# Optimization experiments

Hardware: AMD Instinct MI355X
Metric: run time of the kernel (lower is better)

Reference implementation:

```python
import jax, jax.numpy as jnp
import numpy as np

B, P, D = 256, 128, 768        # batch, property slots per sample, encoder hidden dim
E = 64                          # num_properties (number of adapter heads)
H = 256                         # adapter_hidden_dim
H2 = H // 2
O = 2                           # output_dim
LN_EPS = 1e-5
RES_W_ADPT, RES_W_BASE = 0.7, 0.3


def setup_inputs() -> dict:
    key = jax.random.key(0)
    ks = jax.random.split(key, 12)
    hidden_states = jax.random.normal(ks[0], (B, P, D), dtype=jnp.float32)
    base_output = jax.random.normal(ks[1], (B, P, O), dtype=jnp.float32)
    properties = jax.random.randint(ks[2], (B, P), 0, E, dtype=jnp.int64)
    mask = (jax.random.uniform(ks[3], (B, P)) > 0.1).astype(jnp.float32)
    # Stacked per-head adapter parameters (LayerNorm + 3 Linears per head)
    ln_g = jnp.ones((E, D), dtype=jnp.float32)
    ln_b = jnp.zeros((E, D), dtype=jnp.float32)
    W1 = jax.random.normal(ks[4], (E, D, H), dtype=jnp.float32) * (1.0 / np.sqrt(D))
    b1 = jnp.zeros((E, H), dtype=jnp.float32)
    W2 = jax.random.normal(ks[5], (E, H, H2), dtype=jnp.float32) * (1.0 / np.sqrt(H))
    b2 = jnp.zeros((E, H2), dtype=jnp.float32)
    W3 = jax.random.normal(ks[6], (E, H2, O), dtype=jnp.float32) * 0.01  # init std=0.01 per source
    b3 = jnp.zeros((E, O), dtype=jnp.float32)
    return {
        "hidden_states": hidden_states, "base_output": base_output,
        "properties": properties, "mask": mask,
        "ln_g": ln_g, "ln_b": ln_b, "W1": W1, "b1": b1,
        "W2": W2, "b2": b2, "W3": W3, "b3": b3,
    }


def reference(hidden_states, base_output, properties, mask,
              ln_g, ln_b, W1, b1, W2, b2, W3, b3):
    b, p, d = hidden_states.shape
    o = W3.shape[-1]
    x = hidden_states.reshape(-1, d)                        # [N, D]
    # LayerNorm statistics are head-independent; only gamma/beta differ per head
    mu = jnp.mean(x, axis=-1, keepdims=True)
    var = jnp.mean((x - mu) ** 2, axis=-1, keepdims=True)
    xhat = (x - mu) * jax.lax.rsqrt(var + LN_EPS)           # [N, D]
    flat_p = properties.reshape(-1)                         # [N]
    flat_m = mask.reshape(-1)                               # [N]

    def body(acc, inp):
        idx, g, bt, w1, bb1, w2, bb2, w3, bb3 = inp
        h = jax.nn.relu((xhat * g + bt) @ w1 + bb1)         # [N, H]  (dropout = identity in eval)
        h = jax.nn.relu(h @ w2 + bb2)                       # [N, H2]
        out = h @ w3 + bb3                                  # [N, O]
        sel = (flat_p == idx) & (flat_m > 0)
        return jnp.where(sel[:, None], out, acc), None

    e = W1.shape[0]
    acc0 = jnp.zeros((b * p, o), dtype=x.dtype)
    acc, _ = jax.lax.scan(
        body, acc0,
        (jnp.arange(e), ln_g, ln_b, W1, b1, W2, b2, W3, b3))
    out = acc.reshape(b, p, o)
    out = RES_W_ADPT * out + RES_W_BASE * base_output       # use_residual=True
    return out * mask[..., None]
```

## Files before the change

### kernel.cpp

```cpp
#include <hip/hip_runtime.h>
#include <stdint.h>

typedef unsigned short u16;
typedef unsigned int   u32;

#define NTOK   32768
#define GD     768
#define GH     256
#define GH2    128
#define GE     64

typedef __bf16 bf16x8 __attribute__((ext_vector_type(8)));
typedef float  f32x4  __attribute__((ext_vector_type(4)));
union Frag { uint4 u; bf16x8 b; };

__device__ __forceinline__ float bf2f(u16 h) {
  union { u32 u; float f; } v; v.u = ((u32)h) << 16; return v.f;
}
__device__ __forceinline__ u16 f2bf(float f) {
  union { float f; u32 u; } v; v.f = f;
  u32 r = (v.u + 0x7fffu + ((v.u >> 16) & 1u)) >> 16;
  return (u16)r;
}

__device__ __forceinline__ void async16(void* lds, const void* g) {
  __builtin_amdgcn_global_load_lds(
      (const __attribute__((address_space(1))) void*)g,
      (__attribute__((address_space(3))) void*)lds, 16, 0, 0);
}

__device__ __forceinline__ void bar_lds() {
  asm volatile("s_waitcnt lgkmcnt(0)" ::: "memory");
  __builtin_amdgcn_sched_barrier(0);
  __builtin_amdgcn_s_barrier();
  __builtin_amdgcn_sched_barrier(0);
}

__device__ __forceinline__ int getProp(const int* p32, int t, int is64) {
  return is64 ? p32[2 * t] : p32[t];
}

static const size_t OFF_W1T  = 0;
static const size_t OFF_W2T  = 25165824;
static const size_t OFF_TOK  = 29360128;
static const size_t OFF_META = 29491200;

__global__ void setup_kernel(const int* __restrict__ prop, const float* __restrict__ mask,
                             u32* __restrict__ outz, int* __restrict__ counts2d,
                             int* __restrict__ cursors_p, int* __restrict__ flagp) {
  __shared__ int h[GE];
  __shared__ int vOr;
  const int b = blockIdx.x;
  const int tid = threadIdx.x;
  outz[b * 512 + tid] = 0u;
  outz[b * 512 + 256 + tid] = 0u;
  if (b < 4) cursors_p[b * 256 + tid] = 0;
  if (tid < GE) h[tid] = 0;
  if (tid == 0) vOr = 0;
  __syncthreads();
  int v = prop[2 * tid + 1] | prop[2 * (tid + 256) + 1];
  if (v) atomicOr(&vOr, 1);
  __syncthreads();
  const int is64 = (vOr == 0) ? 1 : 0;
  if (b == 0 && tid == 0) *flagp = is64;
  const int t = b * 256 + tid;
  if (mask[t] > 0.f) atomicAdd(&h[getProp(prop, t, is64)], 1);
  __syncthreads();
  if (tid < GE) counts2d[b * GE + tid] = h[tid];
}

__global__ void transpose_w1(const float* __restrict__ in, u16* __restrict__ out) {
  __shared__ u16 tl[64][260];
  const int bid = blockIdx.x;
  const int e  = bid / 12, r = bid % 12;
  const int d0 = (r / 4) * 256, h0 = (r % 4) * 64;
  const int tid = threadIdx.x;
  const size_t inMat = (size_t)e * GD * GH;
  const size_t outMat = (size_t)e * GH * GD;
  const int h_l = (tid & 15) * 4, d_l = tid >> 4;
#pragma unroll
  for (int dd = 0; dd < 16; ++dd) {
    const int d = d_l + dd * 16;
    float4 v = *(const float4*)(in + inMat + (size_t)(d0 + d) * GH + h0 + h_l);
    tl[h_l + 0][d] = f2bf(v.x);
    tl[h_l + 1][d] = f2bf(v.y);
    tl[h_l + 2][d] = f2bf(v.z);
    tl[h_l + 3][d] = f2bf(v.w);
  }
  __syncthreads();
  const int wv = tid >> 6, ln = tid & 63;
  const int d_glob = d0 + ln * 4;
  const size_t tbase = outMat + (size_t)(d_glob >> 5) * 8192 +
                       (size_t)((d_glob >> 3) & 3) * 2048 + (d_glob & 7);
#pragma unroll
  for (int hh = 0; hh < 16; ++hh) {
    const int h = wv * 16 + hh;
    *(uint2*)(out + tbase + (size_t)(h0 + h) * 8) = *(const uint2*)&tl[h][ln * 4];
  }
}

__global__ void transpose_w2(const float* __restrict__ in, u16* __restrict__ out) {
  __shared__ u16 tile[32][33];
  const int tilesPerMat = 32;
  const int e  = blockIdx.x / tilesPerMat;
  const int t  = blockIdx.x % tilesPerMat;
  const int tr = t / 4, tc = t % 4;
  const size_t mat = (size_t)e * GH * GH2;
  const int tx = threadIdx.x & 31, ty = threadIdx.x >> 5;
  const int r0 = tr * 32, c0 = tc * 32;
#pragma unroll
  for (int i = 0; i < 32; i += 8)
    tile[ty + i][tx] = f2bf(in[mat + (size_t)(r0 + ty + i) * GH2 + c0 + tx]);
  __syncthreads();
  const int k = r0 + tx;
  const size_t kbase = mat + (size_t)(k >> 5) * 4096 +
                       (size_t)((k >> 3) & 3) * 1024 + (k & 7);
#pragma unroll
  for (int i = 0; i < 32; i += 8)
    out[kbase + (size_t)(c0 + ty + i) * 8] = tile[tx][ty + i];
}

__global__ void scan_kernel(const int* __restrict__ counts2d, int* __restrict__ offsets,
                            int* __restrict__ tileHead, int* __restrict__ tileRow,
                            int* __restrict__ nTilesPtr) {
  __shared__ int part[4][GE];
  const int tid = threadIdx.x;
  const int e = tid & 63, q = tid >> 6;
  int c = 0;
  for (int b = q * 32; b < q * 32 + 32; ++b) c += counts2d[b * GE + e];
  part[q][e] = c;
  __syncthreads();
  if (tid < GE) {
    const int ct = part[0][e] + part[1][e] + part[2][e] + part[3][e];
    int inc = ct;
#pragma unroll
    for (int d = 1; d < 64; d <<= 1) { int n = __shfl_up(inc, d); if (e >= d) inc += n; }
    const int off = inc - ct;
    offsets[e] = off;
    if (e == 63) offsets[64] = inc;
    int ntile = (ct + 63) >> 6;
    int inct = ntile;
#pragma unroll
    for (int d = 1; d < 64; d <<= 1) { int n = __shfl_up(inct, d); if (e >= d) inct += n; }
    const int tb = inct - ntile;
    for (int j = 0; j < ntile; ++j) { tileHead[tb + j] = e; tileRow[tb + j] = off + j * 64; }
    if (e == 63) *nTilesPtr = inct;
  }
}

__global__ void scatter_kernel(const int* __restrict__ prop, const float* __restrict__ mask,
                               const int* __restrict__ offsets, int* __restrict__ cursors_p,
                               int* __restrict__ tokenIds, const int* __restrict__ flag) {
  __shared__ int h[GE];
  __shared__ int basebin[GE];
  const int tid = threadIdx.x;
  const int t = blockIdx.x * 256 + tid;
  if (tid < GE) h[tid] = 0;
  __syncthreads();
  int p = -1, rank = 0;
  if (mask[t] > 0.f) {
    p = getProp(prop, t, *flag);
    rank = atomicAdd(&h[p], 1);
  }
  __syncthreads();
  if (tid < GE && h[tid] > 0) basebin[tid] = atomicAdd(&cursors_p[tid * 16], h[tid]);
  __syncthreads();
  if (p >= 0) tokenIds[offsets[p] + basebin[p] + rank] = t;
}

__global__ __launch_bounds__(256, 2) void adapter_gemm(
    const float* __restrict__ hs, const u16* __restrict__ w1t, const u16* __restrict__ w2t,
    const float* __restrict__ lng, const float* __restrict__ lnb,
    const float* __restrict__ b1, const float* __restrict__ b2,
    const float* __restrict__ w3, const float* __restrict__ b3,
    const float* __restrict__ base, const float* __restrict__ mask,
    const int* __restrict__ tokenIds, const int* __restrict__ offsets,
    const int* __restrict__ tileHead, const int* __restrict__ tileRow,
    const int* __restrict__ nTilesPtr, float* __restrict__ outp) {
  __shared__ union LU {
    struct { u16 A[3][2048]; u16 B[3][8192]; } s;
    u16 h[17408];
  } uni;
  __shared__ float sBias1[256];
  __shared__ float sBias2[128];
  __shared__ float sW3[2][128];
  __shared__ float sB3[2];
  __shared__ int   sTok[64];
  __shared__ __align__(16) float sGam[GD];
  __shared__ __align__(16) float sBet[GD];
  __shared__ float sMu[64];
  __shared__ float sRstd[64];

  const int tid  = threadIdx.x;
  const int wv   = tid >> 6;
  const int ln   = tid & 63;
  const int l15  = tid & 15;
  const int quad = (tid & 63) >> 4;
  const f32x4 vzero = {0.f, 0.f, 0.f, 0.f};
  const int nt = *nTilesPtr;
  const int qq = nt >> 3, rr = nt & 7;

  for (int i = blockIdx.x; i < nt; i += gridDim.x) {
    const int x = i & 7, s = i >> 3;
    const int tile = (x < rr ? x * (qq + 1) : rr * (qq + 1) + (x - rr) * qq) + s;

    __syncthreads();
    const int e  = tileHead[tile];
    const int rs = tileRow[tile];
    const int nRows = min(64, offsets[e + 1] - rs);

    if (tid < 64) sTok[tid] = tokenIds[rs + min(tid, nRows - 1)];
    sBias1[tid] = b1[e * GH + tid];
    if (tid < 128) sBias2[tid] = b2[e * GH2 + tid];
    { const int k = tid >> 1, o = tid & 1; sW3[o][k] = w3[e * GH2 * 2 + k * 2 + o]; }
    if (tid < 2) sB3[tid] = b3[e * 2 + tid];
    __syncthreads();

    const u16* w1e = w1t + (size_t)e * GH * GD;
    const u16* w2e = w2t + (size_t)e * GH2 * GH;

    if (tid < 192) {
      *(float4*)&sGam[tid * 4] = *(const float4*)(lng + (size_t)e * GD + tid * 4);
      *(float4*)&sBet[tid * 4] = *(const float4*)(lnb + (size_t)e * GD + tid * 4);
    }

    const int r0  = tid >> 3;
    const int klo = (tid & 7) * 4;
    const int kgrp = klo >> 3, kin = klo & 7;
    const float* xA = hs + (size_t)sTok[r0] * GD + klo;
    const float* xB = hs + (size_t)sTok[r0 + 32] * GD + klo;

#define ISSUE_B(S, KT) do {                                                     \
    u16* _bb = uni.s.B[S] + wv * 2048;                                          \
    const u16* _gg = w1e + (KT) * 8192 + wv * 2048 + ln * 8;                    \
    async16(_bb,        _gg);        async16(_bb + 512,  _gg + 512);            \
    async16(_bb + 1024, _gg + 1024); async16(_bb + 1536, _gg + 1536);           \
  } while (0)

    float4 pAa[2], pAb[2];
    ISSUE_B(0, 0);
    __builtin_amdgcn_sched_barrier(0);
    pAa[0] = *(const float4*)(xA);
    pAb[0] = *(const float4*)(xB);
    ISSUE_B(1, 1);
    __builtin_amdgcn_sched_barrier(0);
    pAa[1] = *(const float4*)(xA + 32);
    pAb[1] = *(const float4*)(xB + 32);

#pragma unroll 2
    for (int pass = 0; pass < 4; ++pass) {
      const int row = pass * 16 + (tid >> 4);
      const int l16 = tid & 15;
      const float* xp = hs + (size_t)sTok[row] * GD + l16 * 4;
      float sm = 0.f, sq = 0.f;
#pragma unroll
      for (int c = 0; c < 12; ++c) {
        float4 u = *(const float4*)(xp + c * 64);
        sm += u.x + u.y + u.z + u.w;
        sq += u.x*u.x + u.y*u.y + u.z*u.z + u.w*u.w;
      }
#pragma unroll
      for (int d = 1; d < 16; d <<= 1) { sm += __shfl_xor(sm, d); sq += __shfl_xor(sq, d); }
      if (l16 == 0) {
        const float mu = sm * (1.f / 768.f);
        sMu[row] = mu;
        sRstd[row] = rsqrtf(sq * (1.f / 768.f) - mu * mu + 1e-5f);
      }
    }
    bar_lds();

    const float muA = sMu[r0],      rsA = sRstd[r0];
    const float muB = sMu[r0 + 32], rsB = sRstd[r0 + 32];

#define XFORM_WRITE(PAR, AA, BB, K0) do {                                       \
    const float4 gv = *(const float4*)&sGam[(K0) + klo];                        \
    const float4 bv = *(const float4*)&sBet[(K0) + klo];                        \
    uint2 oa, ob;                                                               \
    oa.x = (u32)f2bf((AA.x - muA) * rsA * gv.x + bv.x)                          \
         | ((u32)f2bf((AA.y - muA) * rsA * gv.y + bv.y) << 16);                 \
    oa.y = (u32)f2bf((AA.z - muA) * rsA * gv.z + bv.z)                          \
         | ((u32)f2bf((AA.w - muA) * rsA * gv.w + bv.w) << 16);                 \
    ob.x = (u32)f2bf((BB.x - muB) * rsB * gv.x + bv.x)                          \
         | ((u32)f2bf((BB.y - muB) * rsB * gv.y + bv.y) << 16);                 \
    ob.y = (u32)f2bf((BB.z - muB) * rsB * gv.z + bv.z)                          \
         | ((u32)f2bf((BB.w - muB) * rsB * gv.w + bv.w) << 16);                 \
    *(uint2*)&uni.s.A[PAR][kgrp * 512 + r0 * 8 + kin] = oa;                     \
    *(uint2*)&uni.s.A[PAR][kgrp * 512 + (r0 + 32) * 8 + kin] = ob;              \
  } while (0)

    XFORM_WRITE(0, pAa[0], pAb[0], 0);
    bar_lds();

    f32x4 acc1[4][4];
#pragma unroll
    for (int f = 0; f < 4; ++f)
#pragma unroll
      for (int g = 0; g < 4; ++g) acc1[f][g] = vzero;

#pragma unroll
    for (int kt = 0; kt < 24; ++kt) {
      const int par = kt % 3;
      Frag fa[4], fb[4];
#pragma unroll
      for (int f = 0; f < 4; ++f)
        fa[f].u = *(const uint4*)&uni.s.A[par][quad * 512 + (f * 16 + l15) * 8];
#pragma unroll
      for (int g = 0; g < 4; ++g)
        fb[g].u = *(const uint4*)&uni.s.B[par][quad * 2048 + (wv * 64 + g * 16 + l15) * 8];
      if (kt + 2 < 24) {
        ISSUE_B((kt + 2) % 3, kt + 2);
        __builtin_amdgcn_sched_barrier(0);
        pAa[kt & 1] = *(const float4*)(xA + (kt + 2) * 32);
        pAb[kt & 1] = *(const float4*)(xB + (kt + 2) * 32);
      }
#pragma unroll
      for (int f = 0; f < 4; ++f)
#pragma unroll
        for (int g = 0; g < 4; ++g)
          acc1[f][g] = __builtin_amdgcn_mfma_f32_16x16x32_bf16(fa[f].b, fb[g].b, acc1[f][g], 0, 0, 0);
      if (kt + 1 < 24)
        XFORM_WRITE((kt + 1) % 3, pAa[(kt + 1) & 1], pAb[(kt + 1) & 1], (kt + 1) * 32);
      if (kt < 22) {
        asm volatile("s_waitcnt vmcnt(6)" ::: "memory");
      } else {
        asm volatile("s_waitcnt vmcnt(0)" ::: "memory");
      }
      __builtin_amdgcn_sched_barrier(0);
      bar_lds();
    }
    bar_lds();

    Frag bW2[8][2];
#pragma unroll
    for (int kt = 0; kt < 8; ++kt)
#pragma unroll
      for (int g = 0; g < 2; ++g)
        bW2[kt][g].u = *(const uint4*)(w2e + kt * 4096 + quad * 1024 +
                                       (size_t)(wv * 32 + g * 16 + l15) * 8);

#pragma unroll
    for (int f = 0; f < 4; ++f)
#pragma unroll
      for (int g = 0; g < 4; ++g) {
        const int col = wv * 64 + g * 16 + l15;
        const float bias = sBias1[col];
#pragma unroll
        for (int r = 0; r < 4; ++r) {
          const int row = f * 16 + quad * 4 + r;
          uni.h[row * 264 + col] = f2bf(fmaxf(acc1[f][g][r] + bias, 0.f));
        }
      }
    bar_lds();

    f32x4 acc2[4][2];
#pragma unroll
    for (int f = 0; f < 4; ++f)
#pragma unroll
      for (int g = 0; g < 2; ++g) acc2[f][g] = vzero;

#pragma unroll
    for (int kt = 0; kt < 8; ++kt) {
      Frag fa2[4];
#pragma unroll
      for (int f = 0; f < 4; ++f)
        fa2[f].u = *(const uint4*)&uni.h[(f * 16 + l15) * 264 + kt * 32 + quad * 8];
#pragma unroll
      for (int f = 0; f < 4; ++f)
#pragma unroll
        for (int g = 0; g < 2; ++g)
          acc2[f][g] = __builtin_amdgcn_mfma_f32_16x16x32_bf16(fa2[f].b, bW2[kt][g].b, acc2[f][g], 0, 0, 0);
    }
    bar_lds();

#pragma unroll
    for (int f = 0; f < 4; ++f)
#pragma unroll
      for (int g = 0; g < 2; ++g) {
        const int col = wv * 32 + g * 16 + l15;
        const float bias = sBias2[col];
#pragma unroll
        for (int r = 0; r < 4; ++r) {
          const int row = f * 16 + quad * 4 + r;
          uni.h[row * 130 + col] = f2bf(fmaxf(acc2[f][g][r] + bias, 0.f));
        }
      }
    bar_lds();

    const int m = tid >> 1, o = tid & 1;
    if (m < nRows) {
      float a = sB3[o];
      const u16* h2row = &uni.h[m * 130];
#pragma unroll 16
      for (int k = 0; k < 128; ++k) a += bf2f(h2row[k]) * sW3[o][k];
      const int t = sTok[m];
      const float mk = mask[t];
      const float bs = base[t * 2 + o];
      outp[t * 2 + o] = (0.7f * a + 0.3f * bs) * mk;
    }
  }
#undef XFORM_WRITE
#undef ISSUE_B
}

extern "C" void kernel_launch(void* const* d_in, const int* in_sizes, int n_in,
                              void* d_out, int out_size, void* d_ws, size_t ws_size,
                              hipStream_t stream) {
  const float* hs   = (const float*)d_in[0];
  const float* base = (const float*)d_in[1];
  const int*   prop = (const int*)d_in[2];
  const float* mask = (const float*)d_in[3];
  const float* lng  = (const float*)d_in[4];
  const float* lnb  = (const float*)d_in[5];
  const float* W1   = (const float*)d_in[6];
  const float* b1   = (const float*)d_in[7];
  const float* W2   = (const float*)d_in[8];
  const float* b2   = (const float*)d_in[9];
  const float* W3   = (const float*)d_in[10];
  const float* b3   = (const float*)d_in[11];

  char* ws = (char*)d_ws;
  u16* w1t  = (u16*)(ws + OFF_W1T);
  u16* w2t  = (u16*)(ws + OFF_W2T);
  int* tok  = (int*)(ws + OFF_TOK);
  int* meta = (int*)(ws + OFF_META);
  int* counts2d  = meta;
  int* offsets   = meta + 8192;
  int* tileHead  = meta + 8320;
  int* tileRow   = meta + 9344;
  int* nTiles    = meta + 10368;
  int* propFlag  = meta + 10369;
  int* cursors_p = meta + 10432;

  setup_kernel<<<128, 256, 0, stream>>>(prop, mask, (u32*)d_out, counts2d,
                                        cursors_p, propFlag);
  transpose_w1<<<768, 256, 0, stream>>>(W1, w1t);
  transpose_w2<<<64 * 32, 256, 0, stream>>>(W2, w2t);
  scan_kernel<<<1, 256, 0, stream>>>(counts2d, offsets, tileHead, tileRow, nTiles);
  scatter_kernel<<<NTOK / 256, 256, 0, stream>>>(prop, mask, offsets, cursors_p, tok, propFlag);
  adapter_gemm<<<640, 256, 0, stream>>>(hs, w1t, w2t, lng, lnb, b1, b2, W3, b3,
                                        base, mask, tok, offsets, tileHead, tileRow,
                                        nTiles, (float*)d_out);
}
```

Measured before the change: 255.1 us.

## Use 128-row tiles with 512-thread blocks and a deeper W1 prefetch pipeline

Doubles the row tile from 64 to 128 tokens per head, so each W1/W2 weight slice is loaded once per 128 rows instead of per 64. Moves to 8 waves in a 2x4 row/column arrangement with 512-thread blocks, one block per CU, and 320 blocks. Deepens the prefetch pipeline to 4 B stages and 3 register stages for A, adds setprio around the MFMAs, and splits the final W3 dot product across lane pairs. The cost is more padding waste on partial tiles, lower occupancy, and higher LDS use.

```diff
diff --git a/kernel.cpp b/kernel.cpp
--- a/kernel.cpp
+++ b/kernel.cpp
@@ -138,12 +138,12 @@
     const int off = inc - ct;
     offsets[e] = off;
     if (e == 63) offsets[64] = inc;
-    int ntile = (ct + 63) >> 6;
+    int ntile = (ct + 127) >> 7;
     int inct = ntile;
 #pragma unroll
     for (int d = 1; d < 64; d <<= 1) { int n = __shfl_up(inct, d); if (e >= d) inct += n; }
     const int tb = inct - ntile;
-    for (int j = 0; j < ntile; ++j) { tileHead[tb + j] = e; tileRow[tb + j] = off + j * 64; }
+    for (int j = 0; j < ntile; ++j) { tileHead[tb + j] = e; tileRow[tb + j] = off + j * 128; }
     if (e == 63) *nTilesPtr = inct;
   }
 }
@@ -168,7 +168,7 @@
   if (p >= 0) tokenIds[offsets[p] + basebin[p] + rank] = t;
 }
 
-__global__ __launch_bounds__(256, 2) void adapter_gemm(
+__global__ __launch_bounds__(512, 1) void adapter_gemm(
     const float* __restrict__ hs, const u16* __restrict__ w1t, const u16* __restrict__ w2t,
     const float* __restrict__ lng, const float* __restrict__ lnb,
     const float* __restrict__ b1, const float* __restrict__ b2,
@@ -178,21 +178,23 @@
     const int* __restrict__ tileHead, const int* __restrict__ tileRow,
     const int* __restrict__ nTilesPtr, float* __restrict__ outp) {
   __shared__ union LU {
-    struct { u16 A[3][2048]; u16 B[3][8192]; } s;
-    u16 h[17408];
+    struct { u16 A[2][4096]; u16 B[4][8192]; } s;
+    u16 h[33792];
   } uni;
   __shared__ float sBias1[256];
   __shared__ float sBias2[128];
   __shared__ float sW3[2][128];
   __shared__ float sB3[2];
-  __shared__ int   sTok[64];
+  __shared__ int   sTok[128];
   __shared__ __align__(16) float sGam[GD];
   __shared__ __align__(16) float sBet[GD];
-  __shared__ float sMu[64];
-  __shared__ float sRstd[64];
+  __shared__ float sMu[128];
+  __shared__ float sRstd[128];
 
   const int tid  = threadIdx.x;
   const int wv   = tid >> 6;
+  const int wr   = wv >> 2;
+  const int wc   = wv & 3;
   const int ln   = tid & 63;
   const int l15  = tid & 15;
   const int quad = (tid & 63) >> 4;
@@ -207,12 +209,12 @@
     __syncthreads();
     const int e  = tileHead[tile];
     const int rs = tileRow[tile];
-    const int nRows = min(64, offsets[e + 1] - rs);
-
-    if (tid < 64) sTok[tid] = tokenIds[rs + min(tid, nRows - 1)];
-    sBias1[tid] = b1[e * GH + tid];
+    const int nRows = min(128, offsets[e + 1] - rs);
+
+    if (tid < 128) sTok[tid] = tokenIds[rs + min(tid, nRows - 1)];
+    if (tid < 256) sBias1[tid] = b1[e * GH + tid];
     if (tid < 128) sBias2[tid] = b2[e * GH2 + tid];
-    { const int k = tid >> 1, o = tid & 1; sW3[o][k] = w3[e * GH2 * 2 + k * 2 + o]; }
+    if (tid < 256) { const int k = tid >> 1, o = tid & 1; sW3[o][k] = w3[e * GH2 * 2 + k * 2 + o]; }
     if (tid < 2) sB3[tid] = b3[e * 2 + tid];
     __syncthreads();
 
@@ -224,32 +226,30 @@
       *(float4*)&sBet[tid * 4] = *(const float4*)(lnb + (size_t)e * GD + tid * 4);
     }
 
-    const int r0  = tid >> 3;
-    const int klo = (tid & 7) * 4;
-    const int kgrp = klo >> 3, kin = klo & 7;
-    const float* xA = hs + (size_t)sTok[r0] * GD + klo;
-    const float* xB = hs + (size_t)sTok[r0 + 32] * GD + klo;
-
-#define ISSUE_B(S, KT) do {                                                     \
-    u16* _bb = uni.s.B[S] + wv * 2048;                                          \
-    const u16* _gg = w1e + (KT) * 8192 + wv * 2048 + ln * 8;                    \
-    async16(_bb,        _gg);        async16(_bb + 512,  _gg + 512);            \
-    async16(_bb + 1024, _gg + 1024); async16(_bb + 1536, _gg + 1536);           \
+    const int r0x = tid >> 2;
+    const int kg  = tid & 3;
+    const int kg8 = kg * 8;
+    const float* xR = hs + (size_t)sTok[r0x] * GD + kg8;
+
+#define ISSUE_PA(D, KT) do {                                                    \
+    pA[D][0] = *(const float4*)(xR + (KT) * 32);                                \
+    pA[D][1] = *(const float4*)(xR + (KT) * 32 + 4);                            \
   } while (0)
 
-    float4 pAa[2], pAb[2];
+#define ISSUE_B(SB, KT) do {                                                    \
+    u16* _bb = uni.s.B[SB] + wv * 1024;                                         \
+    const u16* _gg = w1e + (KT) * 8192 + wv * 1024 + ln * 8;                    \
+    async16(_bb, _gg); async16(_bb + 512, _gg + 512);                           \
+  } while (0)
+
+    float4 pA[3][2];
+    ISSUE_PA(0, 0);
     ISSUE_B(0, 0);
     __builtin_amdgcn_sched_barrier(0);
-    pAa[0] = *(const float4*)(xA);
-    pAb[0] = *(const float4*)(xB);
-    ISSUE_B(1, 1);
-    __builtin_amdgcn_sched_barrier(0);
-    pAa[1] = *(const float4*)(xA + 32);
-    pAb[1] = *(const float4*)(xB + 32);
 
 #pragma unroll 2
     for (int pass = 0; pass < 4; ++pass) {
-      const int row = pass * 16 + (tid >> 4);
+      const int row = pass * 32 + (tid >> 4);
       const int l16 = tid & 15;
       const float* xp = hs + (size_t)sTok[row] * GD + l16 * 4;
       float sm = 0.f, sq = 0.f;
@@ -267,28 +267,36 @@
         sRstd[row] = rsqrtf(sq * (1.f / 768.f) - mu * mu + 1e-5f);
       }
     }
+    ISSUE_PA(1, 1);
+    ISSUE_B(1, 1);
+    ISSUE_PA(2, 2);
+    ISSUE_B(2, 2);
+    __builtin_amdgcn_sched_barrier(0);
     bar_lds();
 
-    const float muA = sMu[r0],      rsA = sRstd[r0];
-    const float muB = sMu[r0 + 32], rsB = sRstd[r0 + 32];
-
-#define XFORM_WRITE(PAR, AA, BB, K0) do {                                       \
-    const float4 gv = *(const float4*)&sGam[(K0) + klo];                        \
-    const float4 bv = *(const float4*)&sBet[(K0) + klo];                        \
-    uint2 oa, ob;                                                               \
-    oa.x = (u32)f2bf((AA.x - muA) * rsA * gv.x + bv.x)                          \
-         | ((u32)f2bf((AA.y - muA) * rsA * gv.y + bv.y) << 16);                 \
-    oa.y = (u32)f2bf((AA.z - muA) * rsA * gv.z + bv.z)                          \
-         | ((u32)f2bf((AA.w - muA) * rsA * gv.w + bv.w) << 16);                 \
-    ob.x = (u32)f2bf((BB.x - muB) * rsB * gv.x + bv.x)                          \
-         | ((u32)f2bf((BB.y - muB) * rsB * gv.y + bv.y) << 16);                 \
-    ob.y = (u32)f2bf((BB.z - muB) * rsB * gv.z + bv.z)                          \
-         | ((u32)f2bf((BB.w - muB) * rsB * gv.w + bv.w) << 16);                 \
-    *(uint2*)&uni.s.A[PAR][kgrp * 512 + r0 * 8 + kin] = oa;                     \
-    *(uint2*)&uni.s.A[PAR][kgrp * 512 + (r0 + 32) * 8 + kin] = ob;              \
+    const float muR = sMu[r0x], rsR = sRstd[r0x];
+
+#define XFORM_WRITE(PAR, D, K0) do {                                            \
+    const float4 g0 = *(const float4*)&sGam[(K0) + kg8];                        \
+    const float4 g1 = *(const float4*)&sGam[(K0) + kg8 + 4];                    \
+    const float4 bb0 = *(const float4*)&sBet[(K0) + kg8];                       \
+    const float4 bb1 = *(const float4*)&sBet[(K0) + kg8 + 4];                   \
+    const float4 va = pA[D][0], vb = pA[D][1];                                  \
+    uint4 o;                                                                    \
+    o.x = (u32)f2bf((va.x - muR) * rsR * g0.x + bb0.x)                          \
+        | ((u32)f2bf((va.y - muR) * rsR * g0.y + bb0.y) << 16);                 \
+    o.y = (u32)f2bf((va.z - muR) * rsR * g0.z + bb0.z)                          \
+        | ((u32)f2bf((va.w - muR) * rsR * g0.w + bb0.w) << 16);                 \
+    o.z = (u32)f2bf((vb.x - muR) * rsR * g1.x + bb1.x)                          \
+        | ((u32)f2bf((vb.y - muR) * rsR * g1.y + bb1.y) << 16);                 \
+    o.w = (u32)f2bf((vb.z - muR) * rsR * g1.z + bb1.z)                          \
+        | ((u32)f2bf((vb.w - muR) * rsR * g1.w + bb1.w) << 16);                 \
+    *(uint4*)&uni.s.A[PAR][kg * 1024 + r0x * 8] = o;                            \
   } while (0)
 
-    XFORM_WRITE(0, pAa[0], pAb[0], 0);
+    XFORM_WRITE(0, 0, 0);
+    asm volatile("s_waitcnt vmcnt(20)" ::: "memory");
+    __builtin_amdgcn_sched_barrier(0);
     bar_lds();
 
     f32x4 acc1[4][4];
@@ -299,36 +307,37 @@
 
 #pragma unroll
     for (int kt = 0; kt < 24; ++kt) {
-      const int par = kt % 3;
       Frag fa[4], fb[4];
 #pragma unroll
       for (int f = 0; f < 4; ++f)
-        fa[f].u = *(const uint4*)&uni.s.A[par][quad * 512 + (f * 16 + l15) * 8];
+        fa[f].u = *(const uint4*)&uni.s.A[kt & 1][quad * 1024 + (wr * 64 + f * 16 + l15) * 8];
 #pragma unroll
       for (int g = 0; g < 4; ++g)
-        fb[g].u = *(const uint4*)&uni.s.B[par][quad * 2048 + (wv * 64 + g * 16 + l15) * 8];
-      if (kt + 2 < 24) {
-        ISSUE_B((kt + 2) % 3, kt + 2);
+        fb[g].u = *(const uint4*)&uni.s.B[kt & 3][quad * 2048 + (wc * 64 + g * 16 + l15) * 8];
+      if (kt + 3 < 24) {
+        ISSUE_PA((kt + 3) % 3, kt + 3);
+        ISSUE_B((kt + 3) & 3, kt + 3);
         __builtin_amdgcn_sched_barrier(0);
-        pAa[kt & 1] = *(const float4*)(xA + (kt + 2) * 32);
-        pAb[kt & 1] = *(const float4*)(xB + (kt + 2) * 32);
-      }
+      }
+      __builtin_amdgcn_s_setprio(1);
 #pragma unroll
       for (int f = 0; f < 4; ++f)
 #pragma unroll
         for (int g = 0; g < 4; ++g)
           acc1[f][g] = __builtin_amdgcn_mfma_f32_16x16x32_bf16(fa[f].b, fb[g].b, acc1[f][g], 0, 0, 0);
+      __builtin_amdgcn_s_setprio(0);
       if (kt + 1 < 24)
-        XFORM_WRITE((kt + 1) % 3, pAa[(kt + 1) & 1], pAb[(kt + 1) & 1], (kt + 1) * 32);
-      if (kt < 22) {
-        asm volatile("s_waitcnt vmcnt(6)" ::: "memory");
-      } else {
+        XFORM_WRITE((kt + 1) & 1, (kt + 1) % 3, (kt + 1) * 32);
+      if (kt <= 20) {
+        asm volatile("s_waitcnt vmcnt(8)" ::: "memory");
+      } else if (kt == 21) {
+        asm volatile("s_waitcnt vmcnt(4)" ::: "memory");
+      } else if (kt == 22) {
         asm volatile("s_waitcnt vmcnt(0)" ::: "memory");
       }
       __builtin_amdgcn_sched_barrier(0);
       bar_lds();
     }
-    bar_lds();
 
     Frag bW2[8][2];
 #pragma unroll
@@ -336,17 +345,17 @@
 #pragma unroll
       for (int g = 0; g < 2; ++g)
         bW2[kt][g].u = *(const uint4*)(w2e + kt * 4096 + quad * 1024 +
-                                       (size_t)(wv * 32 + g * 16 + l15) * 8);
+                                       (size_t)(wc * 32 + g * 16 + l15) * 8);
 
 #pragma unroll
     for (int f = 0; f < 4; ++f)
 #pragma unroll
       for (int g = 0; g < 4; ++g) {
-        const int col = wv * 64 + g * 16 + l15;
+        const int col = wc * 64 + g * 16 + l15;
         const float bias = sBias1[col];
 #pragma unroll
         for (int r = 0; r < 4; ++r) {
-          const int row = f * 16 + quad * 4 + r;
+          const int row = wr * 64 + f * 16 + quad * 4 + r;
           uni.h[row * 264 + col] = f2bf(fmaxf(acc1[f][g][r] + bias, 0.f));
         }
       }
@@ -363,7 +372,7 @@
       Frag fa2[4];
 #pragma unroll
       for (int f = 0; f < 4; ++f)
-        fa2[f].u = *(const uint4*)&uni.h[(f * 16 + l15) * 264 + kt * 32 + quad * 8];
+        fa2[f].u = *(const uint4*)&uni.h[(wr * 64 + f * 16 + l15) * 264 + kt * 32 + quad * 8];
 #pragma unroll
       for (int f = 0; f < 4; ++f)
 #pragma unroll
@@ -376,29 +385,34 @@
     for (int f = 0; f < 4; ++f)
 #pragma unroll
       for (int g = 0; g < 2; ++g) {
-        const int col = wv * 32 + g * 16 + l15;
+        const int col = wc * 32 + g * 16 + l15;
         const float bias = sBias2[col];
 #pragma unroll
         for (int r = 0; r < 4; ++r) {
-          const int row = f * 16 + quad * 4 + r;
+          const int row = wr * 64 + f * 16 + quad * 4 + r;
           uni.h[row * 130 + col] = f2bf(fmaxf(acc2[f][g][r] + bias, 0.f));
         }
       }
     bar_lds();
 
-    const int m = tid >> 1, o = tid & 1;
-    if (m < nRows) {
-      float a = sB3[o];
-      const u16* h2row = &uni.h[m * 130];
+    {
+      const int m = tid >> 2, o = (tid >> 1) & 1, kh = tid & 1;
+      float a = (kh == 0) ? sB3[o] : 0.f;
+      const u16* h2row = &uni.h[m * 130 + kh * 64];
+      const float* w3row = &sW3[o][kh * 64];
 #pragma unroll 16
-      for (int k = 0; k < 128; ++k) a += bf2f(h2row[k]) * sW3[o][k];
-      const int t = sTok[m];
-      const float mk = mask[t];
-      const float bs = base[t * 2 + o];
-      outp[t * 2 + o] = (0.7f * a + 0.3f * bs) * mk;
+      for (int k = 0; k < 64; ++k) a += bf2f(h2row[k]) * w3row[k];
+      a += __shfl_xor(a, 1);
+      if (kh == 0 && m < nRows) {
+        const int t = sTok[m];
+        const float mk = mask[t];
+        const float bs = base[t * 2 + o];
+        outp[t * 2 + o] = (0.7f * a + 0.3f * bs) * mk;
+      }
     }
   }
 #undef XFORM_WRITE
+#undef ISSUE_PA
 #undef ISSUE_B
 }
 
@@ -437,7 +451,7 @@
   transpose_w2<<<64 * 32, 256, 0, stream>>>(W2, w2t);
   scan_kernel<<<1, 256, 0, stream>>>(counts2d, offsets, tileHead, tileRow, nTiles);
   scatter_kernel<<<NTOK / 256, 256, 0, stream>>>(prop, mask, offsets, cursors_p, tok, propFlag);
-  adapter_gemm<<<640, 256, 0, stream>>>(hs, w1t, w2t, lng, lnb, b1, b2, W3, b3,
+  adapter_gemm<<<320, 512, 0, stream>>>(hs, w1t, w2t, lng, lnb, b1, b2, W3, b3,
                                         base, mask, tok, offsets, tileHead, tileRow,
                                         nTiles, (float*)d_out);
 }
```

New measurement: 263.4 us. 3.3% more time.

## Load W1 fragments directly into registers instead of staging through LDS

Applied to the files above, without the earlier changes.

The W1 B-operand is no longer staged through LDS with async global-to-LDS loads. Each wave now loads its MFMA B fragments straight from global memory into double-buffered registers (even/odd k-tiles), and the activation prefetch is deepened to three stages. This removes LDS traffic and footprint for B and the explicit vmcnt waits, at the cost of more registers and global-load latency that the compiler's waits may expose, since the B fragments are not shared across waves.

```diff
diff --git a/kernel.cpp b/kernel.cpp
--- a/kernel.cpp
+++ b/kernel.cpp
@@ -21,12 +21,6 @@
   union { float f; u32 u; } v; v.f = f;
   u32 r = (v.u + 0x7fffu + ((v.u >> 16) & 1u)) >> 16;
   return (u16)r;
-}
-
-__device__ __forceinline__ void async16(void* lds, const void* g) {
-  __builtin_amdgcn_global_load_lds(
-      (const __attribute__((address_space(1))) void*)g,
-      (__attribute__((address_space(3))) void*)lds, 16, 0, 0);
 }
 
 __device__ __forceinline__ void bar_lds() {
@@ -178,7 +172,7 @@
     const int* __restrict__ tileHead, const int* __restrict__ tileRow,
     const int* __restrict__ nTilesPtr, float* __restrict__ outp) {
   __shared__ union LU {
-    struct { u16 A[3][2048]; u16 B[3][8192]; } s;
+    u16 A[3][2048];
     u16 h[17408];
   } uni;
   __shared__ float sBias1[256];
@@ -193,7 +187,6 @@
 
   const int tid  = threadIdx.x;
   const int wv   = tid >> 6;
-  const int ln   = tid & 63;
   const int l15  = tid & 15;
   const int quad = (tid & 63) >> 4;
   const f32x4 vzero = {0.f, 0.f, 0.f, 0.f};
@@ -230,22 +223,27 @@
     const float* xA = hs + (size_t)sTok[r0] * GD + klo;
     const float* xB = hs + (size_t)sTok[r0 + 32] * GD + klo;
 
-#define ISSUE_B(S, KT) do {                                                     \
-    u16* _bb = uni.s.B[S] + wv * 2048;                                          \
-    const u16* _gg = w1e + (KT) * 8192 + wv * 2048 + ln * 8;                    \
-    async16(_bb,        _gg);        async16(_bb + 512,  _gg + 512);            \
-    async16(_bb + 1024, _gg + 1024); async16(_bb + 1536, _gg + 1536);           \
+    Frag fbE[4], fbO[4];
+#define LOAD_FB(DST, KT) do {                                                   \
+    const u16* _g = w1e + (KT) * 8192 + quad * 2048;                            \
+    DST[0].u = *(const uint4*)(_g + (size_t)(wv * 64 +  0 + l15) * 8);          \
+    DST[1].u = *(const uint4*)(_g + (size_t)(wv * 64 + 16 + l15) * 8);          \
+    DST[2].u = *(const uint4*)(_g + (size_t)(wv * 64 + 32 + l15) * 8);          \
+    DST[3].u = *(const uint4*)(_g + (size_t)(wv * 64 + 48 + l15) * 8);          \
   } while (0)
 
-    float4 pAa[2], pAb[2];
-    ISSUE_B(0, 0);
+#define ISSUE_PA(D, KT) do {                                                    \
+    pA[D][0] = *(const float4*)(xA + (KT) * 32);                                \
+    pA[D][1] = *(const float4*)(xB + (KT) * 32);                                \
+  } while (0)
+
+    float4 pA[3][2];
+    ISSUE_PA(0, 0);
+    ISSUE_PA(1, 1);
+    ISSUE_PA(2, 2);
+    LOAD_FB(fbE, 0);
+    LOAD_FB(fbO, 1);
     __builtin_amdgcn_sched_barrier(0);
-    pAa[0] = *(const float4*)(xA);
-    pAb[0] = *(const float4*)(xB);
-    ISSUE_B(1, 1);
-    __builtin_amdgcn_sched_barrier(0);
-    pAa[1] = *(const float4*)(xA + 32);
-    pAb[1] = *(const float4*)(xB + 32);
 
 #pragma unroll 2
     for (int pass = 0; pass < 4; ++pass) {
@@ -272,23 +270,25 @@
     const float muA = sMu[r0],      rsA = sRstd[r0];
     const float muB = sMu[r0 + 32], rsB = sRstd[r0 + 32];
 
-#define XFORM_WRITE(PAR, AA, BB, K0) do {                                       \
+#define XFORM_WRITE(PAR, D, K0) do {                                            \
     const float4 gv = *(const float4*)&sGam[(K0) + klo];                        \
     const float4 bv = *(const float4*)&sBet[(K0) + klo];                        \
+    const float4 va = pA[D][0], vb = pA[D][1];                                  \
     uint2 oa, ob;                                                               \
-    oa.x = (u32)f2bf((AA.x - muA) * rsA * gv.x + bv.x)                          \
-         | ((u32)f2bf((AA.y - muA) * rsA * gv.y + bv.y) << 16);                 \
-    oa.y = (u32)f2bf((AA.z - muA) * rsA * gv.z + bv.z)                          \
-         | ((u32)f2bf((AA.w - muA) * rsA * gv.w + bv.w) << 16);                 \
-    ob.x = (u32)f2bf((BB.x - muB) * rsB * gv.x + bv.x)                          \
-         | ((u32)f2bf((BB.y - muB) * rsB * gv.y + bv.y) << 16);                 \
-    ob.y = (u32)f2bf((BB.z - muB) * rsB * gv.z + bv.z)                          \
-         | ((u32)f2bf((BB.w - muB) * rsB * gv.w + bv.w) << 16);                 \
-    *(uint2*)&uni.s.A[PAR][kgrp * 512 + r0 * 8 + kin] = oa;                     \
-    *(uint2*)&uni.s.A[PAR][kgrp * 512 + (r0 + 32) * 8 + kin] = ob;              \
+    oa.x = (u32)f2bf((va.x - muA) * rsA * gv.x + bv.x)                          \
+         | ((u32)f2bf((va.y - muA) * rsA * gv.y + bv.y) << 16);                 \
+    oa.y = (u32)f2bf((va.z - muA) * rsA * gv.z + bv.z)                          \
+         | ((u32)f2bf((va.w - muA) * rsA * gv.w + bv.w) << 16);                 \
+    ob.x = (u32)f2bf((vb.x - muB) * rsB * gv.x + bv.x)                          \
+         | ((u32)f2bf((vb.y - muB) * rsB * gv.y + bv.y) << 16);                 \
+    ob.y = (u32)f2bf((vb.z - muB) * rsB * gv.z + bv.z)                          \
+         | ((u32)f2bf((vb.w - muB) * rsB * gv.w + bv.w) << 16);                 \
+    *(uint2*)&uni.A[PAR][kgrp * 512 + r0 * 8 + kin] = oa;                       \
+    *(uint2*)&uni.A[PAR][kgrp * 512 + (r0 + 32) * 8 + kin] = ob;                \
   } while (0)
 
-    XFORM_WRITE(0, pAa[0], pAb[0], 0);
+    XFORM_WRITE(0, 0, 0);
+    XFORM_WRITE(1, 1, 32);
     bar_lds();
 
     f32x4 acc1[4][4];
@@ -299,33 +299,29 @@
 
 #pragma unroll
     for (int kt = 0; kt < 24; ++kt) {
-      const int par = kt % 3;
-      Frag fa[4], fb[4];
+      Frag fa[4];
 #pragma unroll
       for (int f = 0; f < 4; ++f)
-        fa[f].u = *(const uint4*)&uni.s.A[par][quad * 512 + (f * 16 + l15) * 8];
-#pragma unroll
-      for (int g = 0; g < 4; ++g)
-        fb[g].u = *(const uint4*)&uni.s.B[par][quad * 2048 + (wv * 64 + g * 16 + l15) * 8];
-      if (kt + 2 < 24) {
-        ISSUE_B((kt + 2) % 3, kt + 2);
-        __builtin_amdgcn_sched_barrier(0);
-        pAa[kt & 1] = *(const float4*)(xA + (kt + 2) * 32);
-        pAb[kt & 1] = *(const float4*)(xB + (kt + 2) * 32);
+        fa[f].u = *(const uint4*)&uni.A[kt % 3][quad * 512 + (f * 16 + l15) * 8];
+      if ((kt & 1) == 0) {
+#pragma unroll
+        for (int f = 0; f < 4; ++f)
+#pragma unroll
+          for (int g = 0; g < 4; ++g)
+            acc1[f][g] = __builtin_amdgcn_mfma_f32_16x16x32_bf16(fa[f].b, fbE[g].b, acc1[f][g], 0, 0, 0);
+        if (kt + 2 < 24) LOAD_FB(fbE, kt + 2);
+      } else {
+#pragma unroll
+        for (int f = 0; f < 4; ++f)
+#pragma unroll
+          for (int g = 0; g < 4; ++g)
+            acc1[f][g] = __builtin_amdgcn_mfma_f32_16x16x32_bf16(fa[f].b, fbO[g].b, acc1[f][g], 0, 0, 0);
+        if (kt + 2 < 24) LOAD_FB(fbO, kt + 2);
       }
-#pragma unroll
-      for (int f = 0; f < 4; ++f)
-#pragma unroll
-        for (int g = 0; g < 4; ++g)
-          acc1[f][g] = __builtin_amdgcn_mfma_f32_16x16x32_bf16(fa[f].b, fb[g].b, acc1[f][g], 0, 0, 0);
-      if (kt + 1 < 24)
-        XFORM_WRITE((kt + 1) % 3, pAa[(kt + 1) & 1], pAb[(kt + 1) & 1], (kt + 1) * 32);
-      if (kt < 22) {
-        asm volatile("s_waitcnt vmcnt(6)" ::: "memory");
-      } else {
-        asm volatile("s_waitcnt vmcnt(0)" ::: "memory");
-      }
-      __builtin_amdgcn_sched_barrier(0);
+      if (kt + 2 < 24)
+        XFORM_WRITE((kt + 2) % 3, (kt + 2) % 3, (kt + 2) * 32);
+      if (kt + 3 < 24)
+        ISSUE_PA((kt + 3) % 3, kt + 3);
       bar_lds();
     }
     bar_lds();
@@ -399,7 +395,8 @@
     }
   }
 #undef XFORM_WRITE
-#undef ISSUE_B
+#undef ISSUE_PA
+#undef LOAD_FB
 }
 
 extern "C" void kernel_launch(void* const* d_in, const int* in_sizes, int n_in,
```

New measurement: 250.9 us. No clear change (-1.6%).
